# Kernel tuning notes

Measured on AMD Instinct MI355X. Metric: run time of the kernel, lower is better.

The kernel has to match this reference:

```python
import jax, jax.numpy as jnp
import numpy as np

N, C, H, W_SP, E = 32, 64, 128, 128, 512


def setup_inputs() -> dict:
    key = jax.random.key(0)
    k1, k2, k3 = jax.random.split(key, 3)
    images = jax.random.normal(k1, (N, C, H, W_SP), dtype=jnp.float32)
    atts = jax.random.normal(k2, (N, E), dtype=jnp.float32)
    # nn.Linear(E, C*C): weight [C*C, E], bias [C*C]
    W = jax.random.normal(k3, (C * C, E), dtype=jnp.float32) * (1.0 / np.sqrt(E))
    b = jnp.zeros((C * C,), dtype=jnp.float32)
    return {"images": images, "atts": atts, "W": W, "b": b}


def reference(images, atts, W, b):
    n, c, h, w = images.shape
    logits = atts @ W.T + b                      # [N, C*C]
    a = jax.nn.softmax(logits, axis=-1)          # softmax over flattened C*C (first softmax)
    a = a.reshape(n, c, c)
    a = jax.nn.softmax(a, axis=-1)               # second softmax over last C (redundant but faithful)
    # out[n,c,h,w] = sum_d a[n,c,d] * images[n,d,h,w]  (batched [C,C]x[C,HW] matmul)
    out = jnp.einsum('ncd,ndhw->nchw', a, images)
    return out
```

## Files before the change

### kernel.cpp

```cpp
#include <hip/hip_runtime.h>
#include <hip/hip_bf16.h>

#define NB   32
#define CC   64
#define HW   16384
#define EE   512
#define CC2  4096

using short8  = __attribute__((ext_vector_type(8))) short;
using f32x16  = __attribute__((ext_vector_type(16))) float;

__device__ __forceinline__ unsigned short f2bf(float x) {
    unsigned int u = __float_as_uint(x);
    u += 0x7FFFu + ((u >> 16) & 1u);
    return (unsigned short)(u >> 16);
}

__global__ __launch_bounds__(256) void logits_kernel(
    const float* __restrict__ atts, const float* __restrict__ W,
    const float* __restrict__ b, float* __restrict__ logits) {
    const int t  = threadIdx.x;
    const int j  = blockIdx.x * 2 + (t & 1);
    const int n  = (t >> 1) & 31;
    const int kq = t >> 6;
    const float* __restrict__ wrow = W + (size_t)j * EE + kq * 128;
    const float* __restrict__ arow = atts + (size_t)n * EE + kq * 128;
    float acc0 = 0.f, acc1 = 0.f;
    #pragma unroll
    for (int k = 0; k < 128; k += 8) {
        float4 w0 = *reinterpret_cast<const float4*>(wrow + k);
        float4 a0 = *reinterpret_cast<const float4*>(arow + k);
        float4 w1 = *reinterpret_cast<const float4*>(wrow + k + 4);
        float4 a1 = *reinterpret_cast<const float4*>(arow + k + 4);
        acc0 = fmaf(w0.x, a0.x, acc0); acc0 = fmaf(w0.y, a0.y, acc0);
        acc0 = fmaf(w0.z, a0.z, acc0); acc0 = fmaf(w0.w, a0.w, acc0);
        acc1 = fmaf(w1.x, a1.x, acc1); acc1 = fmaf(w1.y, a1.y, acc1);
        acc1 = fmaf(w1.z, a1.z, acc1); acc1 = fmaf(w1.w, a1.w, acc1);
    }
    __shared__ float part[256];
    part[t] = acc0 + acc1;
    __syncthreads();
    if (t < 64) {
        const int jj = blockIdx.x * 2 + (t & 1);
        const int nn = t >> 1;
        const float r = part[t] + part[t + 64] + part[t + 128] + part[t + 192];
        logits[(size_t)nn * CC2 + jj] = r + b[jj];
    }
}

__global__ __launch_bounds__(512) void softmax_kernel(
    const float* __restrict__ logits, unsigned short* __restrict__ a_pk) {
    const int n = blockIdx.x;
    const int t = threadIdx.x;
    __shared__ float s[CC2];
    __shared__ float wred[8];
    __shared__ float rowmx[CC];
    __shared__ float rowis[CC];

    const float* __restrict__ L = logits + (size_t)n * CC2;

    float lmax = -1e30f;
    #pragma unroll
    for (int i = 0; i < 8; ++i) {
        const int idx = t + i * 512;
        float v = L[idx];
        s[idx] = v;
        lmax = fmaxf(lmax, v);
    }
    #pragma unroll
    for (int off = 32; off > 0; off >>= 1) lmax = fmaxf(lmax, __shfl_xor(lmax, off));
    if ((t & 63) == 0) wred[t >> 6] = lmax;
    __syncthreads();
    float bmax = wred[0];
    #pragma unroll
    for (int i = 1; i < 8; ++i) bmax = fmaxf(bmax, wred[i]);

    float lsum = 0.f;
    #pragma unroll
    for (int i = 0; i < 8; ++i) {
        const int idx = t + i * 512;
        float e = __expf(s[idx] - bmax);
        s[idx] = e;
        lsum += e;
    }
    #pragma unroll
    for (int off = 32; off > 0; off >>= 1) lsum += __shfl_xor(lsum, off);
    __syncthreads();
    if ((t & 63) == 0) wred[t >> 6] = lsum;
    __syncthreads();
    float bsum = wred[0];
    #pragma unroll
    for (int i = 1; i < 8; ++i) bsum += wred[i];
    const float inv = 1.f / bsum;

    const int c  = t >> 3;
    const int q8 = (t & 7) * 8;
    const float* __restrict__ row = s + c * CC + q8;

    float v[8];
    #pragma unroll
    for (int i = 0; i < 8; ++i) v[i] = row[i] * inv;

    float mx = v[0];
    #pragma unroll
    for (int i = 1; i < 8; ++i) mx = fmaxf(mx, v[i]);
    mx = fmaxf(mx, __shfl_xor(mx, 1));
    mx = fmaxf(mx, __shfl_xor(mx, 2));
    mx = fmaxf(mx, __shfl_xor(mx, 4));
    float sum = 0.f;
    #pragma unroll
    for (int i = 0; i < 8; ++i) sum += __expf(v[i] - mx);
    sum += __shfl_xor(sum, 1);
    sum += __shfl_xor(sum, 2);
    sum += __shfl_xor(sum, 4);
    const float isum = 1.f / sum;

    union { uint4 u; unsigned short h[8]; } pk;
    #pragma unroll
    for (int i = 0; i < 8; ++i) pk.h[i] = f2bf(__expf(v[i] - mx) * isum);

    const int ks   = q8 >> 4;
    const int lh   = (q8 >> 3) & 1;
    const int half = c >> 5;
    unsigned short* __restrict__ dst =
        a_pk + (size_t)n * CC2 + (size_t)(ks * 2 + half) * 512
             + (lh * 32 + (c & 31)) * 8;
    *reinterpret_cast<uint4*>(dst) = pk.u;
}

__global__ __launch_bounds__(512) void einsum_kernel(
    const float* __restrict__ img, const unsigned short* __restrict__ a_pk,
    float* __restrict__ out) {
    const int t    = threadIdx.x;
    const int lane = t & 63;
    const int wv   = t >> 6;
    const int swz  = blockIdx.x;
    const int bid  = (swz & 7) * 256 + (swz >> 3);
    const int n    = bid >> 6;
    const int px0  = (bid & 63) * 256;
    const int lh   = lane >> 5;
    const int lc   = lane & 31;

    __shared__ unsigned short sImg[CC * 256];

    {
        const int px_l = (t & 63) * 4;
        const int d0   = (t >> 6) * 8;
        const float* __restrict__ gp = img + (size_t)n * (CC * HW) + px0 + px_l;
        float4 v0 = *reinterpret_cast<const float4*>(gp + (size_t)(d0 + 0) * HW);
        float4 v1 = *reinterpret_cast<const float4*>(gp + (size_t)(d0 + 1) * HW);
        float4 v2 = *reinterpret_cast<const float4*>(gp + (size_t)(d0 + 2) * HW);
        float4 v3 = *reinterpret_cast<const float4*>(gp + (size_t)(d0 + 3) * HW);
        float4 v4 = *reinterpret_cast<const float4*>(gp + (size_t)(d0 + 4) * HW);
        float4 v5 = *reinterpret_cast<const float4*>(gp + (size_t)(d0 + 5) * HW);
        float4 v6 = *reinterpret_cast<const float4*>(gp + (size_t)(d0 + 6) * HW);
        float4 v7 = *reinterpret_cast<const float4*>(gp + (size_t)(d0 + 7) * HW);
        union { uint2 u; unsigned short h[4]; } pk;
        #define STG(i, vv) \
            pk.h[0] = f2bf(vv.x); pk.h[1] = f2bf(vv.y); \
            pk.h[2] = f2bf(vv.z); pk.h[3] = f2bf(vv.w); \
            *reinterpret_cast<uint2*>(&sImg[(d0 + i) * 256 + px_l]) = pk.u;
        STG(0, v0) STG(1, v1) STG(2, v2) STG(3, v3)
        STG(4, v4) STG(5, v5) STG(6, v6) STG(7, v7)
        #undef STG
    }
    __syncthreads();

    const int px_w = wv * 32 + lc;
    const unsigned short* __restrict__ apn = a_pk + (size_t)n * CC2;

    f32x16 acc0 = {};
    f32x16 acc1 = {};

    #pragma unroll
    for (int ks = 0; ks < 4; ++ks) {
        const int kbase = ks * 16 + lh * 8;
        union { short8 v; unsigned short h[8]; } bf;
        #pragma unroll
        for (int e = 0; e < 8; ++e)
            bf.h[e] = sImg[(kbase + e) * 256 + px_w];
        short8 a0 = *reinterpret_cast<const short8*>(apn + (ks * 2 + 0) * 512 + lane * 8);
        short8 a1 = *reinterpret_cast<const short8*>(apn + (ks * 2 + 1) * 512 + lane * 8);
        acc0 = __builtin_amdgcn_mfma_f32_32x32x16_bf16(a0, bf.v, acc0, 0, 0, 0);
        acc1 = __builtin_amdgcn_mfma_f32_32x32x16_bf16(a1, bf.v, acc1, 0, 0, 0);
    }

    float* __restrict__ op = out + (size_t)n * (CC * HW) + px0 + px_w;
    #pragma unroll
    for (int r = 0; r < 16; ++r) {
        const int row = (r & 3) + 8 * (r >> 2) + 4 * lh;
        op[(size_t)row * HW]        = acc0[r];
        op[(size_t)(row + 32) * HW] = acc1[r];
    }
}

extern "C" void kernel_launch(void* const* d_in, const int* in_sizes, int n_in,
                              void* d_out, int out_size, void* d_ws, size_t ws_size,
                              hipStream_t stream) {
    const float* images = (const float*)d_in[0];
    const float* atts   = (const float*)d_in[1];
    const float* W      = (const float*)d_in[2];
    const float* b      = (const float*)d_in[3];
    float* out = (float*)d_out;

    float* logits = (float*)d_ws;
    unsigned short* a_pk = (unsigned short*)(logits + NB * CC2);

    logits_kernel<<<CC2 / 2, 256, 0, stream>>>(atts, W, b, logits);
    softmax_kernel<<<NB, 512, 0, stream>>>(logits, a_pk);
    einsum_kernel<<<2048, 512, 0, stream>>>(images, a_pk, out);
}
```

Baseline: 89.24 us.

## Fuse double softmax into einsum kernel, recomputing per block in LDS

Removes the separate softmax kernel. Each einsum block now reads the 4096 logits for its batch, computes both softmaxes itself, and writes the packed bf16 attention matrix to LDS instead of global memory. The image loads are issued before the softmax work so their latency can overlap with it. The cost is that the softmax is recomputed 64 times per batch, LDS use per block grows by about 24KB (which may lower occupancy), and the swizzled block ordering is replaced by a plain 2D grid.

```diff
diff --git a/kernel.cpp b/kernel.cpp
--- a/kernel.cpp
+++ b/kernel.cpp
@@ -48,113 +48,100 @@
     }
 }
 
-__global__ __launch_bounds__(512) void softmax_kernel(
-    const float* __restrict__ logits, unsigned short* __restrict__ a_pk) {
-    const int n = blockIdx.x;
-    const int t = threadIdx.x;
-    __shared__ float s[CC2];
-    __shared__ float wred[8];
-    __shared__ float rowmx[CC];
-    __shared__ float rowis[CC];
-
-    const float* __restrict__ L = logits + (size_t)n * CC2;
-
-    float lmax = -1e30f;
-    #pragma unroll
-    for (int i = 0; i < 8; ++i) {
-        const int idx = t + i * 512;
-        float v = L[idx];
-        s[idx] = v;
-        lmax = fmaxf(lmax, v);
-    }
-    #pragma unroll
-    for (int off = 32; off > 0; off >>= 1) lmax = fmaxf(lmax, __shfl_xor(lmax, off));
-    if ((t & 63) == 0) wred[t >> 6] = lmax;
-    __syncthreads();
-    float bmax = wred[0];
-    #pragma unroll
-    for (int i = 1; i < 8; ++i) bmax = fmaxf(bmax, wred[i]);
-
-    float lsum = 0.f;
-    #pragma unroll
-    for (int i = 0; i < 8; ++i) {
-        const int idx = t + i * 512;
-        float e = __expf(s[idx] - bmax);
-        s[idx] = e;
-        lsum += e;
-    }
-    #pragma unroll
-    for (int off = 32; off > 0; off >>= 1) lsum += __shfl_xor(lsum, off);
-    __syncthreads();
-    if ((t & 63) == 0) wred[t >> 6] = lsum;
-    __syncthreads();
-    float bsum = wred[0];
-    #pragma unroll
-    for (int i = 1; i < 8; ++i) bsum += wred[i];
-    const float inv = 1.f / bsum;
-
-    const int c  = t >> 3;
-    const int q8 = (t & 7) * 8;
-    const float* __restrict__ row = s + c * CC + q8;
-
-    float v[8];
-    #pragma unroll
-    for (int i = 0; i < 8; ++i) v[i] = row[i] * inv;
-
-    float mx = v[0];
-    #pragma unroll
-    for (int i = 1; i < 8; ++i) mx = fmaxf(mx, v[i]);
-    mx = fmaxf(mx, __shfl_xor(mx, 1));
-    mx = fmaxf(mx, __shfl_xor(mx, 2));
-    mx = fmaxf(mx, __shfl_xor(mx, 4));
-    float sum = 0.f;
-    #pragma unroll
-    for (int i = 0; i < 8; ++i) sum += __expf(v[i] - mx);
-    sum += __shfl_xor(sum, 1);
-    sum += __shfl_xor(sum, 2);
-    sum += __shfl_xor(sum, 4);
-    const float isum = 1.f / sum;
-
-    union { uint4 u; unsigned short h[8]; } pk;
-    #pragma unroll
-    for (int i = 0; i < 8; ++i) pk.h[i] = f2bf(__expf(v[i] - mx) * isum);
-
-    const int ks   = q8 >> 4;
-    const int lh   = (q8 >> 3) & 1;
-    const int half = c >> 5;
-    unsigned short* __restrict__ dst =
-        a_pk + (size_t)n * CC2 + (size_t)(ks * 2 + half) * 512
-             + (lh * 32 + (c & 31)) * 8;
-    *reinterpret_cast<uint4*>(dst) = pk.u;
-}
-
 __global__ __launch_bounds__(512) void einsum_kernel(
-    const float* __restrict__ img, const unsigned short* __restrict__ a_pk,
+    const float* __restrict__ img, const float* __restrict__ logits,
     float* __restrict__ out) {
     const int t    = threadIdx.x;
     const int lane = t & 63;
     const int wv   = t >> 6;
-    const int swz  = blockIdx.x;
-    const int bid  = (swz & 7) * 256 + (swz >> 3);
-    const int n    = bid >> 6;
-    const int px0  = (bid & 63) * 256;
+    const int n    = blockIdx.y;
+    const int px0  = blockIdx.x * 256;
     const int lh   = lane >> 5;
     const int lc   = lane & 31;
 
+    __shared__ float s[CC2];
+    __shared__ unsigned short aLds[CC2];
     __shared__ unsigned short sImg[CC * 256];
+    __shared__ float wmax[8];
+    __shared__ float wsum[8];
+
+    const int px_l = (t & 63) * 4;
+    const int d0   = (t >> 6) * 8;
+    const float* __restrict__ gp = img + (size_t)n * (CC * HW) + px0 + px_l;
+    float4 v0 = *reinterpret_cast<const float4*>(gp + (size_t)(d0 + 0) * HW);
+    float4 v1 = *reinterpret_cast<const float4*>(gp + (size_t)(d0 + 1) * HW);
+    float4 v2 = *reinterpret_cast<const float4*>(gp + (size_t)(d0 + 2) * HW);
+    float4 v3 = *reinterpret_cast<const float4*>(gp + (size_t)(d0 + 3) * HW);
+    float4 v4 = *reinterpret_cast<const float4*>(gp + (size_t)(d0 + 4) * HW);
+    float4 v5 = *reinterpret_cast<const float4*>(gp + (size_t)(d0 + 5) * HW);
+    float4 v6 = *reinterpret_cast<const float4*>(gp + (size_t)(d0 + 6) * HW);
+    float4 v7 = *reinterpret_cast<const float4*>(gp + (size_t)(d0 + 7) * HW);
 
     {
-        const int px_l = (t & 63) * 4;
-        const int d0   = (t >> 6) * 8;
-        const float* __restrict__ gp = img + (size_t)n * (CC * HW) + px0 + px_l;
-        float4 v0 = *reinterpret_cast<const float4*>(gp + (size_t)(d0 + 0) * HW);
-        float4 v1 = *reinterpret_cast<const float4*>(gp + (size_t)(d0 + 1) * HW);
-        float4 v2 = *reinterpret_cast<const float4*>(gp + (size_t)(d0 + 2) * HW);
-        float4 v3 = *reinterpret_cast<const float4*>(gp + (size_t)(d0 + 3) * HW);
-        float4 v4 = *reinterpret_cast<const float4*>(gp + (size_t)(d0 + 4) * HW);
-        float4 v5 = *reinterpret_cast<const float4*>(gp + (size_t)(d0 + 5) * HW);
-        float4 v6 = *reinterpret_cast<const float4*>(gp + (size_t)(d0 + 6) * HW);
-        float4 v7 = *reinterpret_cast<const float4*>(gp + (size_t)(d0 + 7) * HW);
+        const float* __restrict__ L = logits + (size_t)n * CC2;
+        float l[8];
+        float lmax = -1e30f;
+        #pragma unroll
+        for (int i = 0; i < 8; ++i) {
+            l[i] = L[t + i * 512];
+            lmax = fmaxf(lmax, l[i]);
+        }
+        #pragma unroll
+        for (int off = 32; off > 0; off >>= 1) lmax = fmaxf(lmax, __shfl_xor(lmax, off));
+        if ((t & 63) == 0) wmax[t >> 6] = lmax;
+        __syncthreads();
+        float bmax = wmax[0];
+        #pragma unroll
+        for (int i = 1; i < 8; ++i) bmax = fmaxf(bmax, wmax[i]);
+
+        float lsum = 0.f;
+        #pragma unroll
+        for (int i = 0; i < 8; ++i) {
+            float e = __expf(l[i] - bmax);
+            s[t + i * 512] = e;
+            lsum += e;
+        }
+        #pragma unroll
+        for (int off = 32; off > 0; off >>= 1) lsum += __shfl_xor(lsum, off);
+        if ((t & 63) == 0) wsum[t >> 6] = lsum;
+        __syncthreads();
+        float bsum = wsum[0];
+        #pragma unroll
+        for (int i = 1; i < 8; ++i) bsum += wsum[i];
+        const float inv = 1.f / bsum;
+
+        const int c  = t >> 3;
+        const int q8 = (t & 7) * 8;
+        const float* __restrict__ row = s + c * CC + q8;
+        float vv[8];
+        #pragma unroll
+        for (int i = 0; i < 8; ++i) vv[i] = row[i] * inv;
+        float mx = vv[0];
+        #pragma unroll
+        for (int i = 1; i < 8; ++i) mx = fmaxf(mx, vv[i]);
+        mx = fmaxf(mx, __shfl_xor(mx, 1));
+        mx = fmaxf(mx, __shfl_xor(mx, 2));
+        mx = fmaxf(mx, __shfl_xor(mx, 4));
+        float sum = 0.f;
+        #pragma unroll
+        for (int i = 0; i < 8; ++i) sum += __expf(vv[i] - mx);
+        sum += __shfl_xor(sum, 1);
+        sum += __shfl_xor(sum, 2);
+        sum += __shfl_xor(sum, 4);
+        const float isum = 1.f / sum;
+
+        union { uint4 u; unsigned short h[8]; } pk;
+        #pragma unroll
+        for (int i = 0; i < 8; ++i) pk.h[i] = f2bf(__expf(vv[i] - mx) * isum);
+
+        const int ks   = q8 >> 4;
+        const int lhp  = (q8 >> 3) & 1;
+        const int half = c >> 5;
+        *reinterpret_cast<uint4*>(
+            &aLds[(size_t)(ks * 2 + half) * 512 + (lhp * 32 + (c & 31)) * 8]) = pk.u;
+    }
+
+    {
         union { uint2 u; unsigned short h[4]; } pk;
         #define STG(i, vv) \
             pk.h[0] = f2bf(vv.x); pk.h[1] = f2bf(vv.y); \
@@ -167,8 +154,6 @@
     __syncthreads();
 
     const int px_w = wv * 32 + lc;
-    const unsigned short* __restrict__ apn = a_pk + (size_t)n * CC2;
-
     f32x16 acc0 = {};
     f32x16 acc1 = {};
 
@@ -179,8 +164,8 @@
         #pragma unroll
         for (int e = 0; e < 8; ++e)
             bf.h[e] = sImg[(kbase + e) * 256 + px_w];
-        short8 a0 = *reinterpret_cast<const short8*>(apn + (ks * 2 + 0) * 512 + lane * 8);
-        short8 a1 = *reinterpret_cast<const short8*>(apn + (ks * 2 + 1) * 512 + lane * 8);
+        short8 a0 = *reinterpret_cast<const short8*>(&aLds[(ks * 2 + 0) * 512 + lane * 8]);
+        short8 a1 = *reinterpret_cast<const short8*>(&aLds[(ks * 2 + 1) * 512 + lane * 8]);
         acc0 = __builtin_amdgcn_mfma_f32_32x32x16_bf16(a0, bf.v, acc0, 0, 0, 0);
         acc1 = __builtin_amdgcn_mfma_f32_32x32x16_bf16(a1, bf.v, acc1, 0, 0, 0);
     }
@@ -204,9 +189,7 @@
     float* out = (float*)d_out;
 
     float* logits = (float*)d_ws;
-    unsigned short* a_pk = (unsigned short*)(logits + NB * CC2);
 
     logits_kernel<<<CC2 / 2, 256, 0, stream>>>(atts, W, b, logits);
-    softmax_kernel<<<NB, 512, 0, stream>>>(logits, a_pk);
-    einsum_kernel<<<2048, 512, 0, stream>>>(images, a_pk, out);
+    einsum_kernel<<<dim3(HW / 256, NB), 512, 0, stream>>>(images, logits, out);
 }
```

New measurement: 83.15 us. -6.8%, faster.
